# Kernel optimization log

Measured on AMD Instinct MI355X. Metric: run time of the kernel, lower is better.

## Reference

```python
import jax, jax.numpy as jnp
import numpy as np

B, C, L = 256, 500, 200
D, H, NUM_ITEMS = 64, 128, 100000
BETA = 0.7
EPS = 1e-8


def _xavier(key, fan_in, fan_out):
    lim = float(np.sqrt(6.0 / (fan_in + fan_out)))
    return jax.random.uniform(key, (fan_in, fan_out), minval=-lim, maxval=lim, dtype=jnp.float32)


def setup_inputs() -> dict:
    key = jax.random.key(0)
    ks = jax.random.split(key, 12)
    inp = {
        'candidate_items': jax.random.randint(ks[0], (B, C), 0, NUM_ITEMS, dtype=jnp.int64) if jax.config.read('jax_enable_x64') else jax.random.randint(ks[0], (B, C), 0, NUM_ITEMS),
        'query_times': jax.random.uniform(ks[1], (B,), dtype=jnp.float32),
        'candidate_histories': jax.random.uniform(ks[2], (B, C, L), dtype=jnp.float32),
        'item_emb': 0.02 * jax.random.normal(ks[3], (NUM_ITEMS, D), dtype=jnp.float32),
        'base_W1': _xavier(ks[4], D, H), 'base_b1': jnp.zeros((H,), jnp.float32),
        'base_W2': _xavier(ks[5], H, H), 'base_b2': jnp.zeros((H,), jnp.float32),
        'base_W3': _xavier(ks[6], H, 1),
        'exc_W1': _xavier(ks[7], D, H), 'exc_b1': jnp.zeros((H,), jnp.float32),
        'exc_W2': _xavier(ks[8], H, H), 'exc_b2': jnp.zeros((H,), jnp.float32),
        'exc_W3': _xavier(ks[9], H, 1),
    }
    return inp


def _mlp(x, W1, b1, W2, b2, W3):
    # (Linear + Softplus) x depth, then Linear -> 1 (no bias), squeeze last dim
    h = jax.nn.softplus(x @ W1 + b1)
    h = jax.nn.softplus(h @ W2 + b2)
    return (h @ W3)[..., 0]


def reference(candidate_items, query_times, candidate_histories, item_emb,
              base_W1, base_b1, base_W2, base_b2, base_W3,
              exc_W1, exc_b1, exc_W2, exc_b2, exc_W3):
    z = item_emb[candidate_items]                                  # [B, C, D]
    mu = jax.nn.softplus(_mlp(z, base_W1, base_b1, base_W2, base_b2, base_W3)) + EPS   # [B, C]
    alpha = jax.nn.softplus(_mlp(z, exc_W1, exc_b1, exc_W2, exc_b2, exc_W3)) + EPS     # [B, C]
    q = query_times[:, None, None]                                 # [B, 1, 1]
    mask = candidate_histories < q                                 # [B, C, L]
    delta = jnp.maximum(q - candidate_histories, 0.0)              # clamp(min=0)
    h = jnp.sum(jnp.exp(-BETA * delta) * mask, axis=-1)            # [B, C]
    return mu + alpha * h
```

## Files before the change

### kernel.cpp

```cpp
#include <hip/hip_runtime.h>
#include <math.h>

#define BB 256
#define CC 500
#define LL 200
#define DD 64
#define HH 128
#define NUM_ITEMS 100000
#define BETA 0.7f
#define EPSV 1e-8f

#define TM 32
#define NTILE (NUM_ITEMS / TM)
#define BPS 1024

typedef _Float16 half8 __attribute__((ext_vector_type(8)));
typedef _Float16 half4 __attribute__((ext_vector_type(4)));
typedef float floatx4 __attribute__((ext_vector_type(4)));

__device__ __forceinline__ float softplus_safe(float x) {
    float t = __expf(-fabsf(x));
    return fmaxf(x, 0.0f) + __logf(1.0f + t);
}
__device__ __forceinline__ float softplus_fast(float x) {
    return __logf(1.0f + __expf(x));
}
__device__ __forceinline__ float softplus_small(float x) {
    float z = x * x;
    float p = fmaf(fmaf(-5.2083333e-3f, z, 0.125f), z, 0.69314718f);
    return fmaf(x, 0.5f, p);
}

__global__ __launch_bounds__(256, 4) void mlp_mfma(
    const float* __restrict__ emb,
    const float* __restrict__ W1, const float* __restrict__ b1,
    const float* __restrict__ W2, const float* __restrict__ b2,
    const float* __restrict__ W3,
    const float* __restrict__ V1, const float* __restrict__ c1,
    const float* __restrict__ V2, const float* __restrict__ c2,
    const float* __restrict__ V3,
    float* __restrict__ mu, float* __restrict__ alpha)
{
    __shared__ __align__(16) _Float16 h1s[TM * HH];
    __shared__ __align__(16) float    part[TM * 4];
    int tid  = threadIdx.x;
    int w    = tid >> 6, lane = tid & 63;
    int quad = lane >> 4, l15 = lane & 15;

    int is_exc = blockIdx.x >= BPS;
    int bslot  = blockIdx.x - (is_exc ? BPS : 0);

    const float* W1s = is_exc ? V1 : W1;
    const float* W2s = is_exc ? V2 : W2;
    const float* B1s = is_exc ? c1 : b1;
    const float* B2s = is_exc ? c2 : b2;
    const float* W3s = is_exc ? V3 : W3;
    float* outp = is_exc ? alpha : mu;

    half8 w1f[2][2];
    half8 w2f[4][2];
    floatx4 b1v[2], b2v[2], w3v[2];
    #pragma unroll
    for (int n = 0; n < 2; ++n) {
        int j  = (2 * w + n) * 16 + l15;
        int cb = (2 * w + n) * 16 + quad * 4;
        #pragma unroll
        for (int r = 0; r < 4; ++r) {
            b1v[n][r] = B1s[cb + r];
            b2v[n][r] = B2s[cb + r];
            w3v[n][r] = W3s[cb + r];
        }
        #pragma unroll
        for (int kt = 0; kt < 2; ++kt) {
            half8 h;
            #pragma unroll
            for (int r = 0; r < 8; ++r)
                h[r] = (_Float16)W1s[(kt * 32 + quad * 8 + r) * HH + j];
            w1f[kt][n] = h;
        }
        #pragma unroll
        for (int kt = 0; kt < 4; ++kt) {
            half8 h;
            #pragma unroll
            for (int r = 0; r < 8; ++r)
                h[r] = (_Float16)W2s[(kt * 32 + quad * 8 + r) * HH + j];
            w2f[kt][n] = h;
        }
    }

    const int wc0  = (2 * w) * 2 + (quad >> 1);
    const int wc1  = (2 * w + 1) * 2 + (quad >> 1);
    const int wsub = (quad & 1) * 4;

    #pragma unroll 1
    for (int t = bslot; t < NTILE; t += BPS) {
        half8 zf[2][2];
        #pragma unroll
        for (int mt = 0; mt < 2; ++mt) {
            const float* p = emb + (size_t)(t * TM + mt * 16 + l15) * DD + quad * 8;
            #pragma unroll
            for (int kt = 0; kt < 2; ++kt) {
                floatx4 v0 = *(const floatx4*)(p + kt * 32);
                floatx4 v1 = *(const floatx4*)(p + kt * 32 + 4);
                half8 z;
                #pragma unroll
                for (int q = 0; q < 4; ++q) {
                    z[q] = (_Float16)v0[q]; z[4 + q] = (_Float16)v1[q];
                }
                zf[mt][kt] = z;
            }
        }

        floatx4 acc1[2][2];
        #pragma unroll
        for (int n = 0; n < 2; ++n)
            #pragma unroll
            for (int mt = 0; mt < 2; ++mt) acc1[mt][n] = b1v[n];
        #pragma unroll
        for (int kt = 0; kt < 2; ++kt)
            #pragma unroll
            for (int n = 0; n < 2; ++n)
                #pragma unroll
                for (int mt = 0; mt < 2; ++mt)
                    acc1[mt][n] = __builtin_amdgcn_mfma_f32_16x16x32_f16(
                        w1f[kt][n], zf[mt][kt], acc1[mt][n], 0, 0, 0);
        #pragma unroll
        for (int mt = 0; mt < 2; ++mt)
            #pragma unroll
            for (int n = 0; n < 2; ++n) {
                half4 hv;
                #pragma unroll
                for (int r = 0; r < 4; ++r)
                    hv[r] = (_Float16)softplus_small(acc1[mt][n][r]);
                int wc = n ? wc1 : wc0;
                *(half4*)(&h1s[(mt * 16 + l15) * HH + ((wc ^ l15) * 8) + wsub]) = hv;
            }
        __syncthreads();

        floatx4 acc2[2][2];
        #pragma unroll
        for (int n = 0; n < 2; ++n)
            #pragma unroll
            for (int mt = 0; mt < 2; ++mt) acc2[mt][n] = b2v[n];
        #pragma unroll
        for (int kt = 0; kt < 4; ++kt) {
            half8 af[2];
            #pragma unroll
            for (int mt = 0; mt < 2; ++mt)
                af[mt] = *(const half8*)(&h1s[(mt * 16 + l15) * HH +
                                              (((kt * 4 + quad) ^ l15) * 8)]);
            #pragma unroll
            for (int n = 0; n < 2; ++n)
                #pragma unroll
                for (int mt = 0; mt < 2; ++mt)
                    acc2[mt][n] = __builtin_amdgcn_mfma_f32_16x16x32_f16(
                        w2f[kt][n], af[mt], acc2[mt][n], 0, 0, 0);
        }
        #pragma unroll
        for (int mt = 0; mt < 2; ++mt) {
            float sv = 0.0f;
            #pragma unroll
            for (int n = 0; n < 2; ++n)
                #pragma unroll
                for (int r = 0; r < 4; ++r)
                    sv = fmaf(softplus_fast(acc2[mt][n][r]), w3v[n][r], sv);
            sv += __shfl_xor(sv, 16, 64);
            sv += __shfl_xor(sv, 32, 64);
            if (quad == 0)
                part[(mt * 16 + l15) * 4 + w] = sv;
        }
        __syncthreads();

        if (tid < TM) {
            floatx4 pv = *(const floatx4*)(part + tid * 4);
            float s = (pv[0] + pv[1]) + (pv[2] + pv[3]);
            outp[t * TM + tid] = softplus_safe(s) + EPSV;
        }
    }
}

__global__ __launch_bounds__(256) void hawkes_kernel(
    const int* __restrict__ items,
    const float* __restrict__ qt,
    const float* __restrict__ hist,
    const float* __restrict__ mu,
    const float* __restrict__ alpha,
    float* __restrict__ out)
{
    int w = blockIdx.x * 4 + (threadIdx.x >> 6);
    int lane = threadIdx.x & 63;
    float q = qt[w / CC];

    float s = 0.0f;
    if (lane < LL / 4) {
        float4 v = *(const float4*)(hist + (size_t)w * LL + lane * 4);
        s  = (v.x < q) ? __expf(BETA * v.x) : 0.f;
        s += (v.y < q) ? __expf(BETA * v.y) : 0.f;
        s += (v.z < q) ? __expf(BETA * v.z) : 0.f;
        s += (v.w < q) ? __expf(BETA * v.w) : 0.f;
    }
    #pragma unroll
    for (int off = 1; off < 64; off <<= 1) s += __shfl_xor(s, off, 64);

    if (lane == 0) {
        int it = items[w];
        out[w] = fmaf(alpha[it] * __expf(-BETA * q), s, mu[it]);
    }
}

extern "C" void kernel_launch(void* const* d_in, const int* in_sizes, int n_in,
                              void* d_out, int out_size, void* d_ws, size_t ws_size,
                              hipStream_t stream)
{
    const int*   items = (const int*)  d_in[0];
    const float* qt    = (const float*)d_in[1];
    const float* hist  = (const float*)d_in[2];
    const float* emb   = (const float*)d_in[3];
    const float* W1    = (const float*)d_in[4];
    const float* b1    = (const float*)d_in[5];
    const float* W2    = (const float*)d_in[6];
    const float* b2    = (const float*)d_in[7];
    const float* W3    = (const float*)d_in[8];
    const float* V1    = (const float*)d_in[9];
    const float* c1    = (const float*)d_in[10];
    const float* V2    = (const float*)d_in[11];
    const float* c2    = (const float*)d_in[12];
    const float* V3    = (const float*)d_in[13];

    float* out   = (float*)d_out;
    float* mu    = (float*)d_ws;
    float* alpha = mu + NUM_ITEMS;

    mlp_mfma<<<2 * BPS, 256, 0, stream>>>(emb, W1, b1, W2, b2, W3,
                                          V1, c1, V2, c2, V3, mu, alpha);

    hawkes_kernel<<<(BB * CC) / 4, 256, 0, stream>>>(items, qt, hist, mu, alpha, out);
}
```

Before: 238.1 us.

## Overlap history reduction with MLP in one launch and add gather-combine kernel

The history exponential-sum reduction moves into the same launch as the MFMA MLP, with two of every three blocks reducing history rows and the third running MLP tiles. This lets the memory-bound history stream overlap the compute-bound MLP. A small combine kernel then gathers interleaved mu/alpha pairs per item and writes the output. The change also switches fp16 conversions to packed cvt_pkrtz and uses nontemporal loads for the history. In exchange it adds a round trip to workspace for the per-row sums.

```diff
diff --git a/kernel.cpp b/kernel.cpp
--- a/kernel.cpp
+++ b/kernel.cpp
@@ -13,9 +13,14 @@
 #define TM 32
 #define NTILE (NUM_ITEMS / TM)
 #define BPS 1024
+#define NB_MLP (2 * BPS)
+#define NB_HWK 4096
+#define NB_ALL (NB_MLP + NB_HWK)
+#define NROW (BB * CC)
 
 typedef _Float16 half8 __attribute__((ext_vector_type(8)));
 typedef _Float16 half4 __attribute__((ext_vector_type(4)));
+typedef __fp16   pk2   __attribute__((ext_vector_type(2)));
 typedef float floatx4 __attribute__((ext_vector_type(4)));
 
 __device__ __forceinline__ float softplus_safe(float x) {
@@ -31,7 +36,7 @@
     return fmaf(x, 0.5f, p);
 }
 
-__global__ __launch_bounds__(256, 4) void mlp_mfma(
+__global__ __launch_bounds__(256, 4) void fused(
     const float* __restrict__ emb,
     const float* __restrict__ W1, const float* __restrict__ b1,
     const float* __restrict__ W2, const float* __restrict__ b2,
@@ -39,23 +44,50 @@
     const float* __restrict__ V1, const float* __restrict__ c1,
     const float* __restrict__ V2, const float* __restrict__ c2,
     const float* __restrict__ V3,
-    float* __restrict__ mu, float* __restrict__ alpha)
+    const float* __restrict__ qt,
+    const float* __restrict__ hist,
+    float* __restrict__ ma2,
+    float* __restrict__ spart)
 {
     __shared__ __align__(16) _Float16 h1s[TM * HH];
     __shared__ __align__(16) float    part[TM * 4];
+    int bid  = blockIdx.x;
     int tid  = threadIdx.x;
     int w    = tid >> 6, lane = tid & 63;
+
+    if (bid % 3 != 2) {
+        int hslot = bid - bid / 3;
+        #pragma unroll 1
+        for (int r = hslot * 4 + w; r < NROW; r += NB_HWK * 4) {
+            float q = qt[r / CC];
+            float s = 0.0f;
+            if (lane < LL / 4) {
+                const floatx4* hp = (const floatx4*)(hist + (size_t)r * LL) + lane;
+                floatx4 v = __builtin_nontemporal_load(hp);
+                s  = (v[0] < q) ? __expf(BETA * v[0]) : 0.f;
+                s += (v[1] < q) ? __expf(BETA * v[1]) : 0.f;
+                s += (v[2] < q) ? __expf(BETA * v[2]) : 0.f;
+                s += (v[3] < q) ? __expf(BETA * v[3]) : 0.f;
+            }
+            #pragma unroll
+            for (int off = 1; off < 64; off <<= 1) s += __shfl_xor(s, off, 64);
+            if (lane == 0)
+                spart[r] = s * __expf(-BETA * q);
+        }
+        return;
+    }
+
+    int mslot  = bid / 3;
     int quad = lane >> 4, l15 = lane & 15;
 
-    int is_exc = blockIdx.x >= BPS;
-    int bslot  = blockIdx.x - (is_exc ? BPS : 0);
+    int is_exc = mslot >= BPS;
+    int bslot  = mslot - (is_exc ? BPS : 0);
 
     const float* W1s = is_exc ? V1 : W1;
     const float* W2s = is_exc ? V2 : W2;
     const float* B1s = is_exc ? c1 : b1;
     const float* B2s = is_exc ? c2 : b2;
     const float* W3s = is_exc ? V3 : W3;
-    float* outp = is_exc ? alpha : mu;
 
     half8 w1f[2][2];
     half8 w2f[4][2];
@@ -102,12 +134,12 @@
             for (int kt = 0; kt < 2; ++kt) {
                 floatx4 v0 = *(const floatx4*)(p + kt * 32);
                 floatx4 v1 = *(const floatx4*)(p + kt * 32 + 4);
-                half8 z;
-                #pragma unroll
-                for (int q = 0; q < 4; ++q) {
-                    z[q] = (_Float16)v0[q]; z[4 + q] = (_Float16)v1[q];
-                }
-                zf[mt][kt] = z;
+                union { half8 h; pk2 p2[4]; } u;
+                u.p2[0] = __builtin_amdgcn_cvt_pkrtz(v0[0], v0[1]);
+                u.p2[1] = __builtin_amdgcn_cvt_pkrtz(v0[2], v0[3]);
+                u.p2[2] = __builtin_amdgcn_cvt_pkrtz(v1[0], v1[1]);
+                u.p2[3] = __builtin_amdgcn_cvt_pkrtz(v1[2], v1[3]);
+                zf[mt][kt] = u.h;
             }
         }
 
@@ -128,12 +160,13 @@
         for (int mt = 0; mt < 2; ++mt)
             #pragma unroll
             for (int n = 0; n < 2; ++n) {
-                half4 hv;
-                #pragma unroll
-                for (int r = 0; r < 4; ++r)
-                    hv[r] = (_Float16)softplus_small(acc1[mt][n][r]);
+                union { half4 h; pk2 p2[2]; } hu;
+                hu.p2[0] = __builtin_amdgcn_cvt_pkrtz(
+                    softplus_small(acc1[mt][n][0]), softplus_small(acc1[mt][n][1]));
+                hu.p2[1] = __builtin_amdgcn_cvt_pkrtz(
+                    softplus_small(acc1[mt][n][2]), softplus_small(acc1[mt][n][3]));
                 int wc = n ? wc1 : wc0;
-                *(half4*)(&h1s[(mt * 16 + l15) * HH + ((wc ^ l15) * 8) + wsub]) = hv;
+                *(half4*)(&h1s[(mt * 16 + l15) * HH + ((wc ^ l15) * 8) + wsub]) = hu.h;
             }
         __syncthreads();
 
@@ -174,38 +207,21 @@
         if (tid < TM) {
             floatx4 pv = *(const floatx4*)(part + tid * 4);
             float s = (pv[0] + pv[1]) + (pv[2] + pv[3]);
-            outp[t * TM + tid] = softplus_safe(s) + EPSV;
+            ma2[2 * (t * TM + tid) + is_exc] = softplus_safe(s) + EPSV;
         }
     }
 }
 
-__global__ __launch_bounds__(256) void hawkes_kernel(
+__global__ __launch_bounds__(256) void combine_kernel(
     const int* __restrict__ items,
-    const float* __restrict__ qt,
-    const float* __restrict__ hist,
-    const float* __restrict__ mu,
-    const float* __restrict__ alpha,
+    const float* __restrict__ ma2,
+    const float* __restrict__ spart,
     float* __restrict__ out)
 {
-    int w = blockIdx.x * 4 + (threadIdx.x >> 6);
-    int lane = threadIdx.x & 63;
-    float q = qt[w / CC];
-
-    float s = 0.0f;
-    if (lane < LL / 4) {
-        float4 v = *(const float4*)(hist + (size_t)w * LL + lane * 4);
-        s  = (v.x < q) ? __expf(BETA * v.x) : 0.f;
-        s += (v.y < q) ? __expf(BETA * v.y) : 0.f;
-        s += (v.z < q) ? __expf(BETA * v.z) : 0.f;
-        s += (v.w < q) ? __expf(BETA * v.w) : 0.f;
-    }
-    #pragma unroll
-    for (int off = 1; off < 64; off <<= 1) s += __shfl_xor(s, off, 64);
-
-    if (lane == 0) {
-        int it = items[w];
-        out[w] = fmaf(alpha[it] * __expf(-BETA * q), s, mu[it]);
-    }
+    int w = blockIdx.x * 256 + threadIdx.x;
+    int it = items[w];
+    float2 g = *(const float2*)(ma2 + 2 * it);
+    out[w] = fmaf(g.y, spart[w], g.x);
 }
 
 extern "C" void kernel_launch(void* const* d_in, const int* in_sizes, int n_in,
@@ -228,11 +244,12 @@
     const float* V3    = (const float*)d_in[13];
 
     float* out   = (float*)d_out;
-    float* mu    = (float*)d_ws;
-    float* alpha = mu + NUM_ITEMS;
-
-    mlp_mfma<<<2 * BPS, 256, 0, stream>>>(emb, W1, b1, W2, b2, W3,
-                                          V1, c1, V2, c2, V3, mu, alpha);
-
-    hawkes_kernel<<<(BB * CC) / 4, 256, 0, stream>>>(items, qt, hist, mu, alpha, out);
-}
+    float* ma2   = (float*)d_ws;
+    float* spart = ma2 + 2 * NUM_ITEMS;
+
+    fused<<<NB_ALL, 256, 0, stream>>>(emb, W1, b1, W2, b2, W3,
+                                      V1, c1, V2, c2, V3,
+                                      qt, hist, ma2, spart);
+
+    combine_kernel<<<NROW / 256, 256, 0, stream>>>(items, ma2, spart, out);
+}
```

New measurement: 244.9 us. 1.03x slower.
